# Kernel tuning notes

Measured on AMD Instinct MI355X. Metric: run time of the kernel, lower is better.

## Reference

```python
import jax, jax.numpy as jnp
import numpy as np

D_MODEL = 512
D_INNER = 1024   # expand=2
D_STATE = 16
D_CONV = 4
DT_RANK = 32     # ceil(d_model/16)
N_LAYERS = 3
STATE_DIM = 256
NUM_ACTIONS = 9
BATCH = 8
SEQ = 1024


def setup_inputs() -> dict:
    key = jax.random.key(0)
    ks = iter(jax.random.split(key, 32))
    def nrm(shape, scale=0.02):
        return jax.random.normal(next(ks), shape, jnp.float32) * scale
    inp = {}
    inp["state_sequences"] = jax.random.normal(next(ks), (BATCH, SEQ, STATE_DIM), jnp.float32)
    inp["embed_w"] = nrm((D_MODEL, STATE_DIM), STATE_DIM ** -0.5)
    inp["embed_b"] = jnp.zeros((D_MODEL,), jnp.float32)
    inp["in_proj_w"] = nrm((N_LAYERS, 2 * D_INNER, D_MODEL), D_MODEL ** -0.5)
    inp["conv_w"] = nrm((N_LAYERS, D_INNER, D_CONV), 0.2)
    inp["conv_b"] = jnp.zeros((N_LAYERS, D_INNER), jnp.float32)
    inp["x_proj_w"] = nrm((N_LAYERS, DT_RANK + 2 * D_STATE, D_INNER), D_INNER ** -0.5)
    inp["dt_proj_w"] = nrm((N_LAYERS, D_INNER, DT_RANK), DT_RANK ** -0.5)
    # bias so that softplus(dt) ~ 0.01 (standard mamba dt init)
    inp["dt_proj_b"] = jnp.full((N_LAYERS, D_INNER), float(np.log(np.expm1(0.01))), jnp.float32)
    # S4D-real init: A_n = n for n = 1..d_state
    inp["A_log"] = jnp.log(jnp.broadcast_to(
        jnp.arange(1, D_STATE + 1, dtype=jnp.float32), (N_LAYERS, D_INNER, D_STATE)))
    inp["D"] = jnp.ones((N_LAYERS, D_INNER), jnp.float32)
    inp["out_proj_w"] = nrm((N_LAYERS, D_MODEL, D_INNER), D_INNER ** -0.5)
    inp["head1_w"] = nrm((D_MODEL // 2, D_MODEL), D_MODEL ** -0.5)
    inp["head1_b"] = jnp.zeros((D_MODEL // 2,), jnp.float32)
    inp["head2_w"] = nrm((NUM_ACTIONS, D_MODEL // 2), (D_MODEL // 2) ** -0.5)
    inp["head2_b"] = jnp.zeros((NUM_ACTIONS,), jnp.float32)
    return inp


def _mamba_block(x, in_w, cw, cb, xw, dtw, dtb, A_log, Dp, ow):
    """One mamba-ssm Mamba layer (d_inner=2*d_model, d_state=16, d_conv=4)."""
    B, L, _ = x.shape
    xz = jnp.einsum('bld,ed->ble', x, in_w)            # (B,L,2*d_inner)
    xi, z = jnp.split(xz, 2, axis=-1)
    # causal depthwise conv1d along time
    xc = jnp.pad(xi, ((0, 0), (D_CONV - 1, 0), (0, 0)))
    conv = jax.lax.conv_general_dilated(
        xc.transpose(0, 2, 1), cw[:, None, :], (1,), 'VALID',
        feature_group_count=D_INNER)                   # (B,d_inner,L)
    xi = jax.nn.silu(conv.transpose(0, 2, 1) + cb)     # (B,L,d_inner)
    dbl = jnp.einsum('bld,ed->ble', xi, xw)            # (B,L,dt_rank+2*d_state)
    dt, Bm, Cm = jnp.split(dbl, [DT_RANK, DT_RANK + D_STATE], axis=-1)
    dt = jax.nn.softplus(jnp.einsum('blr,dr->bld', dt, dtw) + dtb)  # (B,L,d_inner)
    A = -jnp.exp(A_log)                                # (d_inner,d_state)

    def step(h, inputs):
        dt_t, x_t, B_t, C_t = inputs                   # (B,di),(B,di),(B,ds),(B,ds)
        dA = jnp.exp(dt_t[:, :, None] * A)             # (B,di,ds)
        h = dA * h + (dt_t * x_t)[:, :, None] * B_t[:, None, :]
        y_t = jnp.einsum('bds,bs->bd', h, C_t)
        return h, y_t

    h0 = jnp.zeros((B, D_INNER, D_STATE), xi.dtype)
    seq = (dt.transpose(1, 0, 2), xi.transpose(1, 0, 2),
           Bm.transpose(1, 0, 2), Cm.transpose(1, 0, 2))
    _, ys = jax.lax.scan(step, h0, seq)                # (L,B,d_inner)
    y = ys.transpose(1, 0, 2) + xi * Dp
    y = y * jax.nn.silu(z)
    return jnp.einsum('bld,ed->ble', y, ow)            # (B,L,d_model)


def reference(state_sequences, embed_w, embed_b, in_proj_w, conv_w, conv_b,
              x_proj_w, dt_proj_w, dt_proj_b, A_log, D, out_proj_w,
              head1_w, head1_b, head2_w, head2_b):
    x = jnp.einsum('bls,ds->bld', state_sequences, embed_w) + embed_b
    for i in range(N_LAYERS):
        x = _mamba_block(x, in_proj_w[i], conv_w[i], conv_b[i], x_proj_w[i],
                         dt_proj_w[i], dt_proj_b[i], A_log[i], D[i], out_proj_w[i])
    h = jax.nn.relu(jnp.einsum('bd,hd->bh', x[:, -1, :], head1_w) + head1_b)
    logits = jnp.einsum('bh,ah->ba', h, head2_w) + head2_b  # (B,num_actions)
    return logits
```

## Files before the change

### kernel.cpp

```cpp
#include <hip/hip_runtime.h>
#include <cstdint>
#include <cstddef>


#define DEVI static __device__ __forceinline__

using short8 = __attribute__((ext_vector_type(8))) short;
using f32x4  = __attribute__((ext_vector_type(4))) float;
typedef unsigned short ushort;
typedef unsigned int uint;

extern "C" __device__ float __ocml_native_exp2_f32(float);
DEVI float exp2n_(float x) { return __ocml_native_exp2_f32(x); }

DEVI float sigmoidf_(float x) { return 1.f / (1.f + __expf(-x)); }
DEVI float siluf_(float x)    { return x * sigmoidf_(x); }
DEVI float softplusf_(float x){ return fmaxf(x, 0.f) + log1pf(expf(-fabsf(x))); }

DEVI ushort rne_bf16(float f) {
    uint u = __float_as_uint(f);
    return (ushort)((u + 0x7fffu + ((u >> 16) & 1u)) >> 16);
}
DEVI float bf16_to_f(ushort h) { return __uint_as_float(((uint)h) << 16); }
DEVI uint pack_hl(float v) {
    const ushort hv = rne_bf16(v);
    const ushort lv = rne_bf16(v - bf16_to_f(hv));
    return (uint)hv | ((uint)lv << 16);
}

DEVI void swz_block(int& bx, int& by, int gx, int gy) {
    const int total = gx * gy;
    const int q = total >> 3;
    const int id = by * gx + bx;
    const int s = (id & 7) * q + (id >> 3);
    bx = s % gx;
    by = s / gx;
}

constexpr int LC = 32;
constexpr int NC = 32;
constexpr int PF = 4;
constexpr float LOG2E = 1.44269504f;

DEVI void cvt4(const float4 v, ushort* h, ushort* l) {
    const float vv[4] = {v.x, v.y, v.z, v.w};
    #pragma unroll
    for (int e = 0; e < 4; e++) {
        const ushort hh = rne_bf16(vv[e]);
        h[e] = hh;
        l[e] = rne_bf16(vv[e] - bf16_to_f(hh));
    }
}

__global__ __launch_bounds__(256)
void wcvt_gi_kernel(const float* __restrict__ src, ushort* __restrict__ hi,
                    ushort* __restrict__ lo, int N, int K)
{
    const int idx = blockIdx.x * 256 + threadIdx.x;
    if (idx >= N * (K >> 3)) return;
    const int g = idx / N;
    const int n = idx - g * N;
    const float4 v0 = *reinterpret_cast<const float4*>(&src[(size_t)n * K + g * 8]);
    const float4 v1 = *reinterpret_cast<const float4*>(&src[(size_t)n * K + g * 8 + 4]);
    ushort h[8], l[8];
    cvt4(v0, h, l);
    cvt4(v1, h + 4, l + 4);
    short8 h8, l8;
    #pragma unroll
    for (int e = 0; e < 8; e++) { h8[e] = (short)h[e]; l8[e] = (short)l[e]; }
    *reinterpret_cast<short8*>(&hi[(size_t)idx * 8]) = h8;
    *reinterpret_cast<short8*>(&lo[(size_t)idx * 8]) = l8;
}

__global__ __launch_bounds__(256)
void wcvt3_kernel(const float* __restrict__ s_in, const float* __restrict__ s_out,
                  const float* __restrict__ s_xp, ushort* __restrict__ dst)
{
    const int idx = blockIdx.x * 256 + threadIdx.x;
    if (idx >= 212992) return;
    if (idx < 131072) {
        const int g = idx >> 11, n = idx & 2047;
        const float* sp = s_in + (size_t)n * 512 + g * 8;
        const float4 v0 = *reinterpret_cast<const float4*>(sp);
        const float4 v1 = *reinterpret_cast<const float4*>(sp + 4);
        ushort h[8], l[8];
        cvt4(v0, h, l); cvt4(v1, h + 4, l + 4);
        short8 h8, l8;
        #pragma unroll
        for (int e = 0; e < 8; e++) { h8[e] = (short)h[e]; l8[e] = (short)l[e]; }
        *reinterpret_cast<short8*>(&dst[(size_t)idx * 8]) = h8;
        *reinterpret_cast<short8*>(&dst[1048576 + (size_t)idx * 8]) = l8;
    } else if (idx < 196608) {
        const int j = idx - 131072;
        const int g = j >> 9, n = j & 511;
        const float* sp = s_out + (size_t)n * 1024 + g * 8;
        const float4 v0 = *reinterpret_cast<const float4*>(sp);
        const float4 v1 = *reinterpret_cast<const float4*>(sp + 4);
        ushort h[8], l[8];
        cvt4(v0, h, l); cvt4(v1, h + 4, l + 4);
        short8 h8, l8;
        #pragma unroll
        for (int e = 0; e < 8; e++) { h8[e] = (short)h[e]; l8[e] = (short)l[e]; }
        *reinterpret_cast<short8*>(&dst[2097152 + (size_t)j * 8]) = h8;
        *reinterpret_cast<short8*>(&dst[2621440 + (size_t)j * 8]) = l8;
    } else {
        const int j = idx - 196608;
        const int loc = j * 4;
        const float4 v = *reinterpret_cast<const float4*>(&s_xp[loc]);
        ushort h[4], l[4];
        cvt4(v, h, l);
        *reinterpret_cast<ushort4*>(&dst[3145728 + loc]) = make_ushort4(h[0], h[1], h[2], h[3]);
        *reinterpret_cast<ushort4*>(&dst[3211264 + loc]) = make_ushort4(l[0], l[1], l[2], l[3]);
    }
}

template<int ACT, int AMODE, bool OPACK>
__global__ __launch_bounds__(256)
void gemm_mfma(const float* __restrict__ A, const uint* __restrict__ Apk,
               int lda,
               const ushort* __restrict__ Whi, const ushort* __restrict__ Wlo,
               int Wn, const float* __restrict__ bias,
               float* C, float* C2, int nsplit,
               uint* __restrict__ Cpk, int ldc, int K)
{
    __shared__ short As_hi[4096], As_lo[4096];

    int bx = blockIdx.x, by = blockIdx.y;
    swz_block(bx, by, gridDim.x, gridDim.y);

    const int tid  = threadIdx.x;
    const int lane = tid & 63;
    const int wave = tid >> 6;
    const int wr   = wave >> 1;
    const int wc   = wave & 1;
    const int row0 = by * 128;
    const int col0 = bx * 128;

    const int g  = tid & 3;
    const int r0 = tid >> 2;

    const int lg = lane >> 4;
    const int lm = lane & 15;
    const int chA = lg * 128 + ((wr * 64 + lm) ^ lg);

    f32x4 acc[4][4];
    #pragma unroll
    for (int i = 0; i < 4; i++)
        #pragma unroll
        for (int j = 0; j < 4; j++) acc[i][j] = (f32x4){0.f, 0.f, 0.f, 0.f};

    float4 av0[2], av1[2];
    uint4  au0[2], au1[2];

    auto gloadA = [&](int k0) {
        #pragma unroll
        for (int p = 0; p < 2; p++) {
            const int rr = r0 + p * 64;
            if constexpr (AMODE == 1) {
                const uint* ap = Apk + (size_t)(row0 + rr) * lda + k0 + g * 8;
                au0[p] = *reinterpret_cast<const uint4*>(ap);
                au1[p] = *reinterpret_cast<const uint4*>(ap + 4);
            } else {
                const float* ap = A + (size_t)(row0 + rr) * lda + k0 + g * 8;
                av0[p] = *reinterpret_cast<const float4*>(ap);
                av1[p] = *reinterpret_cast<const float4*>(ap + 4);
            }
        }
    };

    gloadA(0);

    for (int k0 = 0; k0 < K; k0 += 32) {
        #pragma unroll
        for (int p = 0; p < 2; p++) {
            const int ch = g * 128 + ((r0 + p * 64) ^ g);
            short8 h8, l8;
            if constexpr (AMODE == 1) {
                uint u[8];
                *reinterpret_cast<uint4*>(u)     = au0[p];
                *reinterpret_cast<uint4*>(u + 4) = au1[p];
                uint* hp = reinterpret_cast<uint*>(&h8);
                uint* lp = reinterpret_cast<uint*>(&l8);
                #pragma unroll
                for (int e = 0; e < 4; e++) {
                    hp[e] = __builtin_amdgcn_perm(u[2*e+1], u[2*e], 0x05040100u);
                    lp[e] = __builtin_amdgcn_perm(u[2*e+1], u[2*e], 0x07060302u);
                }
            } else {
                ushort h[8], l[8];
                cvt4(av0[p], h, l);
                cvt4(av1[p], h + 4, l + 4);
                #pragma unroll
                for (int e = 0; e < 8; e++) { h8[e] = (short)h[e]; l8[e] = (short)l[e]; }
            }
            *reinterpret_cast<short8*>(&As_hi[ch * 8]) = h8;
            *reinterpret_cast<short8*>(&As_lo[ch * 8]) = l8;
        }
        if (k0 + 32 < K) gloadA(k0 + 32);

        short8 b_hi[4], b_lo[4];
        {
            const size_t gkb = (size_t)((k0 >> 3) + lg) * Wn + col0 + wc * 64 + lm;
            #pragma unroll
            for (int j = 0; j < 4; j++) {
                const size_t wo = (gkb + j * 16) * 8;
                b_hi[j] = *reinterpret_cast<const short8*>(&Whi[wo]);
                b_lo[j] = *reinterpret_cast<const short8*>(&Wlo[wo]);
            }
        }
        __syncthreads();

        short8 a_hi[4], a_lo[4];
        #pragma unroll
        for (int i = 0; i < 4; i++) {
            a_hi[i] = *reinterpret_cast<const short8*>(&As_hi[(chA + i * 16) * 8]);
            a_lo[i] = *reinterpret_cast<const short8*>(&As_lo[(chA + i * 16) * 8]);
        }
        #pragma unroll
        for (int i = 0; i < 4; i++)
            #pragma unroll
            for (int j = 0; j < 4; j++) {
                acc[i][j] = __builtin_amdgcn_mfma_f32_16x16x32_bf16(a_hi[i], b_hi[j], acc[i][j], 0, 0, 0);
                acc[i][j] = __builtin_amdgcn_mfma_f32_16x16x32_bf16(a_hi[i], b_lo[j], acc[i][j], 0, 0, 0);
                acc[i][j] = __builtin_amdgcn_mfma_f32_16x16x32_bf16(a_lo[i], b_hi[j], acc[i][j], 0, 0, 0);
            }
        __syncthreads();
    }

    float* Cw = C;
    int cofs = 0;
    if (C2 != nullptr && col0 >= nsplit) { Cw = C2; cofs = nsplit; }

    #pragma unroll
    for (int i = 0; i < 4; i++) {
        const int grow = row0 + wr * 64 + i * 16 + lg * 4;
        #pragma unroll
        for (int j = 0; j < 4; j++) {
            const int gcol = col0 + wc * 64 + j * 16 + lm;
            float bv = 0.f;
            if constexpr (ACT >= 1) bv = bias[gcol];
            #pragma unroll
            for (int r = 0; r < 4; r++) {
                const float v = acc[i][j][r] + bv;
                if constexpr (OPACK) {
                    Cpk[(size_t)(grow + r) * ldc + gcol] = pack_hl(v);
                } else {
                    Cw[(size_t)(grow + r) * ldc + (gcol - cofs)] = v;
                }
            }
        }
    }
}

__global__ __launch_bounds__(256)
void gemm_mfma_xp(const float* __restrict__ A,
                  const ushort* __restrict__ Whi,
                  const ushort* __restrict__ Wlo,
                  float* __restrict__ P)
{
    __shared__ short As_hi[2048], As_lo[2048], Ws_hi[2048], Ws_lo[2048];

    int bx = blockIdx.x, by = blockIdx.y;
    swz_block(bx, by, gridDim.x, gridDim.y);

    const int tid  = threadIdx.x;
    const int lane = tid & 63;
    const int wave = tid >> 6;
    const int wr   = wave >> 1;
    const int wc   = wave & 1;
    const int row0 = bx * 64;
    const int kp   = by;

    const int g = tid & 3;
    const int r = tid >> 2;
    const int ch_st = g * 64 + (r ^ g);

    const int lg = lane >> 4;
    const int lm = lane & 15;

    f32x4 acc[2][2];
    #pragma unroll
    for (int i = 0; i < 2; i++)
        #pragma unroll
        for (int j = 0; j < 2; j++) acc[i][j] = (f32x4){0.f, 0.f, 0.f, 0.f};

    for (int ks = 0; ks < 4; ks++) {
        const int kbase = kp * 128 + ks * 32;
        __syncthreads();
        {
            const float* ap = A + (size_t)(row0 + r) * 1024 + kbase + g * 8;
            const float4 v0 = *reinterpret_cast<const float4*>(ap);
            const float4 v1 = *reinterpret_cast<const float4*>(ap + 4);
            ushort h[8], l[8];
            cvt4(v0, h, l);
            cvt4(v1, h + 4, l + 4);
            short8 h8, l8;
            #pragma unroll
            for (int e = 0; e < 8; e++) { h8[e] = (short)h[e]; l8[e] = (short)l[e]; }
            *reinterpret_cast<short8*>(&As_hi[ch_st * 8]) = h8;
            *reinterpret_cast<short8*>(&As_lo[ch_st * 8]) = l8;
        }
        {
            const size_t wo = (size_t)r * 1024 + kbase + g * 8;
            *reinterpret_cast<short8*>(&Ws_hi[ch_st * 8]) =
                *reinterpret_cast<const short8*>(&Whi[wo]);
            *reinterpret_cast<short8*>(&Ws_lo[ch_st * 8]) =
                *reinterpret_cast<const short8*>(&Wlo[wo]);
        }
        __syncthreads();

        short8 a_hi[2], a_lo[2], b_hi[2], b_lo[2];
        #pragma unroll
        for (int i = 0; i < 2; i++) {
            const int ch = lg * 64 + ((wr * 32 + i * 16 + lm) ^ lg);
            a_hi[i] = *reinterpret_cast<const short8*>(&As_hi[ch * 8]);
            a_lo[i] = *reinterpret_cast<const short8*>(&As_lo[ch * 8]);
        }
        #pragma unroll
        for (int j = 0; j < 2; j++) {
            const int ch = lg * 64 + ((wc * 32 + j * 16 + lm) ^ lg);
            b_hi[j] = *reinterpret_cast<const short8*>(&Ws_hi[ch * 8]);
            b_lo[j] = *reinterpret_cast<const short8*>(&Ws_lo[ch * 8]);
        }
        #pragma unroll
        for (int i = 0; i < 2; i++)
            #pragma unroll
            for (int j = 0; j < 2; j++) {
                acc[i][j] = __builtin_amdgcn_mfma_f32_16x16x32_bf16(a_hi[i], b_hi[j], acc[i][j], 0, 0, 0);
                acc[i][j] = __builtin_amdgcn_mfma_f32_16x16x32_bf16(a_hi[i], b_lo[j], acc[i][j], 0, 0, 0);
                acc[i][j] = __builtin_amdgcn_mfma_f32_16x16x32_bf16(a_lo[i], b_hi[j], acc[i][j], 0, 0, 0);
            }
    }

    #pragma unroll
    for (int i = 0; i < 2; i++) {
        const int grow = row0 + wr * 32 + i * 16 + lg * 4;
        #pragma unroll
        for (int j = 0; j < 2; j++) {
            const int gcol = wc * 32 + j * 16 + lm;
            #pragma unroll
            for (int rr = 0; rr < 4; rr++)
                P[((size_t)kp * 8192 + grow + rr) * 64 + gcol] = acc[i][j][rr];
        }
    }
}

__global__ __launch_bounds__(256)
void xp_reduce(const float* __restrict__ P, float* __restrict__ dbl)
{
    const int idx = blockIdx.x * 256 + threadIdx.x;
    float s = 0.f;
    #pragma unroll
    for (int p = 0; p < 8; p++) s += P[(size_t)p * 524288 + idx];
    dbl[idx] = s;
}

__global__ __launch_bounds__(256)
void conv_silu_kernel(const float* __restrict__ xpre,
                      const float* __restrict__ cw,
                      const float* __restrict__ cb,
                      float* __restrict__ xi)
{
    const int idx = blockIdx.x * 256 + threadIdx.x;
    const int d = idx & 1023;
    const int l = (idx >> 10) & 1023;
    const int b = idx >> 20;

    const float4 w = reinterpret_cast<const float4*>(cw)[d];
    float acc = cb[d];
    const float* base = xpre + (size_t)b * 1024 * 1024 + d;
    if (l >= 3) acc = fmaf(base[(size_t)(l - 3) * 1024], w.x, acc);
    if (l >= 2) acc = fmaf(base[(size_t)(l - 2) * 1024], w.y, acc);
    if (l >= 1) acc = fmaf(base[(size_t)(l - 1) * 1024], w.z, acc);
    acc = fmaf(base[(size_t)l * 1024], w.w, acc);
    xi[idx] = siluf_(acc);
}

__global__ __launch_bounds__(256)
void dt_kernel(const float* __restrict__ dbl,
               const float* __restrict__ dtw,
               const float* __restrict__ dtb,
               float* __restrict__ dtout)
{
    __shared__ float S[LC][32];
    const int tid = threadIdx.x;
    const int d   = blockIdx.x * 256 + tid;
    const int c   = blockIdx.y;
    const int b   = blockIdx.z;
    const int t0  = c * LC;

    {
        const int t = tid >> 3, q = tid & 7;
        *reinterpret_cast<float4*>(&S[t][q * 4]) =
            *reinterpret_cast<const float4*>(&dbl[((size_t)b * 1024 + t0 + t) * 64 + q * 4]);
    }
    __syncthreads();

    float W[32];
    #pragma unroll
    for (int q = 0; q < 8; q++)
        *reinterpret_cast<float4*>(&W[q * 4]) =
            *reinterpret_cast<const float4*>(&dtw[(size_t)d * 32 + q * 4]);
    const float bias = dtb[d];

    float* dto = dtout + ((size_t)b * 1024 + t0) * 1024 + d;
    #pragma unroll 4
    for (int t = 0; t < LC; t++) {
        float a0 = bias, a1 = 0.f, a2 = 0.f, a3 = 0.f;
        #pragma unroll
        for (int q = 0; q < 8; q += 4) {
            const float4 s0 = *reinterpret_cast<const float4*>(&S[t][q * 4]);
            const float4 s1 = *reinterpret_cast<const float4*>(&S[t][q * 4 + 4]);
            a0 = fmaf(W[q*4+0], s0.x, a0); a1 = fmaf(W[q*4+1], s0.y, a1);
            a2 = fmaf(W[q*4+2], s0.z, a2); a3 = fmaf(W[q*4+3], s0.w, a3);
            a0 = fmaf(W[q*4+4], s1.x, a0); a1 = fmaf(W[q*4+5], s1.y, a1);
            a2 = fmaf(W[q*4+6], s1.z, a2); a3 = fmaf(W[q*4+7], s1.w, a3);
        }
        dto[(size_t)t * 1024] = softplusf_((a0 + a1) + (a2 + a3));
    }
}

__global__ __launch_bounds__(256)
void scan_p1(const float* __restrict__ xi,
             const float* __restrict__ dtin,
             const float* __restrict__ dbl,
             const float* __restrict__ A_log,
             float* __restrict__ hend,
             float* __restrict__ dtsum)
{
    __shared__ float S[LC][16];
    const int tid  = threadIdx.x;
    const int lane = tid & 63;
    const int wave = tid >> 6;
    const int dloc = lane & 31;
    const int half = lane >> 5;
    const int d    = blockIdx.x * 128 + wave * 32 + dloc;
    const int c    = blockIdx.y;
    const int b    = blockIdx.z;
    const int t0   = c * LC;

    if (tid < 128) {
        const int t = tid >> 2, q = tid & 3;
        *reinterpret_cast<float4*>(&S[t][q * 4]) =
            *reinterpret_cast<const float4*>(&dbl[((size_t)b * 1024 + t0 + t) * 64 + 32 + q * 4]);
    }
    __syncthreads();

    const float A2b = -__expf(A_log[d * 16]) * LOG2E;
    float h[8];
    #pragma unroll
    for (int s = 0; s < 8; s++) h[s] = 0.f;
    float dts = 0.f;

    const float* xi_p = xi   + ((size_t)b * 1024 + t0) * 1024 + d;
    const float* dt_p = dtin + ((size_t)b * 1024 + t0) * 1024 + d;

    float x0[PF], d0[PF], x1[PF], d1[PF], x2[PF], d2[PF];

    auto load = [&](int bt, float (&nx)[PF], float (&nd)[PF]) {
        #pragma unroll
        for (int j = 0; j < PF; j++) {
            const size_t tt = (size_t)(bt * PF + j);
            nx[j] = xi_p[tt * 1024];
            nd[j] = dt_p[tt * 1024];
        }
    };
    auto comp = [&](int bt, float (&cx)[PF], float (&cd)[PF]) {
        #pragma unroll
        for (int j = 0; j < PF; j++) {
            const int t = bt * PF + j;
            const float dtv = cd[j];
            dts += dtv;
            const float dx = dtv * cx[j];
            const float E  = exp2n_(dtv * A2b);
            const float E2 = E * E;
            const float E4 = E2 * E2;
            const float E8 = E4 * E4;
            float p = half ? E8 * E : E;
            const float4 B0 = *reinterpret_cast<const float4*>(&S[t][half * 8]);
            const float4 B1 = *reinterpret_cast<const float4*>(&S[t][half * 8 + 4]);
            h[0] = fmaf(p, h[0], dx * B0.x); p *= E;
            h[1] = fmaf(p, h[1], dx * B0.y); p *= E;
            h[2] = fmaf(p, h[2], dx * B0.z); p *= E;
            h[3] = fmaf(p, h[3], dx * B0.w); p *= E;
            h[4] = fmaf(p, h[4], dx * B1.x); p *= E;
            h[5] = fmaf(p, h[5], dx * B1.y); p *= E;
            h[6] = fmaf(p, h[6], dx * B1.z); p *= E;
            h[7] = fmaf(p, h[7], dx * B1.w);
        }
    };

    load(0, x0, d0); load(1, x1, d1);
    load(2, x2, d2); comp(0, x0, d0);
    load(3, x0, d0); comp(1, x1, d1);
    load(4, x1, d1); comp(2, x2, d2);
    load(5, x2, d2); comp(3, x0, d0);
    load(6, x0, d0); comp(4, x1, d1);
    load(7, x1, d1); comp(5, x2, d2);
    comp(6, x0, d0);
    comp(7, x1, d1);

    float* hp = hend + (((size_t)b * NC + c) * 1024 + d) * 16 + half * 8;
    *reinterpret_cast<float4*>(&hp[0]) = *reinterpret_cast<const float4*>(&h[0]);
    *reinterpret_cast<float4*>(&hp[4]) = *reinterpret_cast<const float4*>(&h[4]);
    if (half == 0) dtsum[((size_t)b * NC + c) * 1024 + d] = dts;
}

__global__ __launch_bounds__(256)
void scan_p2(float* __restrict__ hbuf,
             const float* __restrict__ dtsum,
             const float* __restrict__ A_log)
{
    const int gid = blockIdx.x * 256 + threadIdx.x;
    const int s = gid & 15;
    const int d = (gid >> 4) & 1023;
    const int b = gid >> 14;

    const float A2 = -__expf(A_log[d * 16 + s]) * LOG2E;
    float h = 0.f;
    #pragma unroll
    for (int c = 0; c < NC; c++) {
        const size_t idx = (((size_t)b * NC + c) * 1024 + d) * 16 + s;
        const float he = hbuf[idx];
        const float aP = exp2n_(A2 * dtsum[((size_t)b * NC + c) * 1024 + d]);
        hbuf[idx] = h;
        h = fmaf(aP, h, he);
    }
}

__global__ __launch_bounds__(256)
void scan_p3(const float* __restrict__ xi,
             float* dtio,
             const float* __restrict__ dbl,
             const float* __restrict__ zbuf,
             const float* __restrict__ A_log,
             const float* __restrict__ Dp,
             const float* __restrict__ h0)
{
    __shared__ float S[LC][32];
    const int tid  = threadIdx.x;
    const int lane = tid & 63;
    const int wave = tid >> 6;
    const int dloc = lane & 31;
    const int half = lane >> 5;
    const int d    = blockIdx.x * 128 + wave * 32 + dloc;
    const int c    = blockIdx.y;
    const int b    = blockIdx.z;
    const int t0   = c * LC;

    {
        const int t = tid >> 3, q = tid & 7;
        *reinterpret_cast<float4*>(&S[t][q * 4]) =
            *reinterpret_cast<const float4*>(&dbl[((size_t)b * 1024 + t0 + t) * 64 + 32 + q * 4]);
    }
    __syncthreads();

    const float A2b = -__expf(A_log[d * 16]) * LOG2E;
    float h[8];
    const float* h0p = h0 + (((size_t)b * NC + c) * 1024 + d) * 16 + half * 8;
    *reinterpret_cast<float4*>(&h[0]) = *reinterpret_cast<const float4*>(&h0p[0]);
    *reinterpret_cast<float4*>(&h[4]) = *reinterpret_cast<const float4*>(&h0p[4]);

    const float Dv = Dp[d];
    const size_t rowbase = ((size_t)b * 1024 + t0) * 1024 + d;
    const float* xi_p = xi + rowbase;
    const float* dt_p = dtio + rowbase;
    const float* z_p  = zbuf + rowbase;
    uint* ypk_p = reinterpret_cast<uint*>(dtio) + rowbase;

    float x0[PF], z0[PF], d0[PF], x1[PF], z1[PF], d1[PF], x2[PF], z2[PF], d2[PF];

    auto load = [&](int bt, float (&nx)[PF], float (&nz)[PF], float (&nd)[PF]) {
        #pragma unroll
        for (int j = 0; j < PF; j++) {
            const size_t tt = (size_t)(bt * PF + j);
            nx[j] = xi_p[tt * 1024];
            nz[j] = z_p[tt * 1024];
            nd[j] = dt_p[tt * 1024];
        }
    };
    auto comp = [&](int bt, float (&cx)[PF], float (&cz)[PF], float (&cd)[PF]) {
        #pragma unroll
        for (int j = 0; j < PF; j++) {
            const int t = bt * PF + j;
            const float dtv = cd[j];
            const float dx  = dtv * cx[j];
            const float E  = exp2n_(dtv * A2b);
            const float E2 = E * E;
            const float E4 = E2 * E2;
            const float E8 = E4 * E4;
            float p = half ? E8 * E : E;
            const float4 B0 = *reinterpret_cast<const float4*>(&S[t][half * 8]);
            const float4 B1 = *reinterpret_cast<const float4*>(&S[t][half * 8 + 4]);
            const float4 C0 = *reinterpret_cast<const float4*>(&S[t][16 + half * 8]);
            const float4 C1 = *reinterpret_cast<const float4*>(&S[t][16 + half * 8 + 4]);
            float y = 0.f;
            h[0] = fmaf(p, h[0], dx * B0.x); y = fmaf(h[0], C0.x, y); p *= E;
            h[1] = fmaf(p, h[1], dx * B0.y); y = fmaf(h[1], C0.y, y); p *= E;
            h[2] = fmaf(p, h[2], dx * B0.z); y = fmaf(h[2], C0.z, y); p *= E;
            h[3] = fmaf(p, h[3], dx * B0.w); y = fmaf(h[3], C0.w, y); p *= E;
            h[4] = fmaf(p, h[4], dx * B1.x); y = fmaf(h[4], C1.x, y); p *= E;
            h[5] = fmaf(p, h[5], dx * B1.y); y = fmaf(h[5], C1.y, y); p *= E;
            h[6] = fmaf(p, h[6], dx * B1.z); y = fmaf(h[6], C1.z, y); p *= E;
            h[7] = fmaf(p, h[7], dx * B1.w); y = fmaf(h[7], C1.w, y);
            const float yfull = y + __shfl_xor(y, 32);
            if (half == 0) {
                const float yv = (yfull + cx[j] * Dv) * siluf_(cz[j]);
                ypk_p[(size_t)t * 1024] = pack_hl(yv);
            }
        }
    };

    load(0, x0, z0, d0); load(1, x1, z1, d1);
    load(2, x2, z2, d2); comp(0, x0, z0, d0);
    load(3, x0, z0, d0); comp(1, x1, z1, d1);
    load(4, x1, z1, d1); comp(2, x2, z2, d2);
    load(5, x2, z2, d2); comp(3, x0, z0, d0);
    load(6, x0, z0, d0); comp(4, x1, z1, d1);
    load(7, x1, z1, d1); comp(5, x2, z2, d2);
    comp(6, x0, z0, d0);
    comp(7, x1, z1, d1);
}

__global__ __launch_bounds__(256)
void head1_kernel(const uint* __restrict__ xpk,
                  const float* __restrict__ w,
                  const float* __restrict__ bias,
                  float* __restrict__ hh)
{
    const int tid = threadIdx.x;
    const int jl  = tid >> 4;
    const int ks  = tid & 15;
    const int j   = blockIdx.x * 16 + jl;

    const float* wr = w + (size_t)j * 512 + ks * 32;
    float acc[8];
    #pragma unroll
    for (int b = 0; b < 8; b++) {
        const size_t ro = ((size_t)b * 1024 + 1023) * 512 + ks * 32;
        float a = 0.f;
        #pragma unroll
        for (int k = 0; k < 32; k += 4) {
            const float4 wv = *reinterpret_cast<const float4*>(&wr[k]);
            const uint4  pv = *reinterpret_cast<const uint4*>(&xpk[ro + k]);
            a = fmaf(wv.x, bf16_to_f((ushort)(pv.x & 0xffff)) + bf16_to_f((ushort)(pv.x >> 16)), a);
            a = fmaf(wv.y, bf16_to_f((ushort)(pv.y & 0xffff)) + bf16_to_f((ushort)(pv.y >> 16)), a);
            a = fmaf(wv.z, bf16_to_f((ushort)(pv.z & 0xffff)) + bf16_to_f((ushort)(pv.z >> 16)), a);
            a = fmaf(wv.w, bf16_to_f((ushort)(pv.w & 0xffff)) + bf16_to_f((ushort)(pv.w >> 16)), a);
        }
        acc[b] = a;
    }
    #pragma unroll
    for (int b = 0; b < 8; b++) {
        float p = acc[b];
        p += __shfl_xor(p, 1);
        p += __shfl_xor(p, 2);
        p += __shfl_xor(p, 4);
        p += __shfl_xor(p, 8);
        if (ks == 0) hh[b * 256 + j] = fmaxf(p + bias[j], 0.f);
    }
}

__global__ void head2_kernel(const float* __restrict__ hh,
                             const float* __restrict__ w,
                             const float* __restrict__ b2,
                             float* __restrict__ out)
{
    const int t = threadIdx.x;
    if (t < 72) {
        const int bb = t / 9, a = t % 9;
        const float* hr = hh + bb * 256;
        const float* wr = w + a * 256;
        float acc = b2[a];
        for (int jj = 0; jj < 256; jj++) acc = fmaf(hr[jj], wr[jj], acc);
        out[t] = acc;
    }
}


extern "C" void kernel_launch(void* const* d_in, const int* in_sizes, int n_in,
                              void* d_out, int out_size, void* d_ws, size_t ws_size,
                              hipStream_t stream)
{
    const float* state     = (const float*)d_in[0];
    const float* embed_w   = (const float*)d_in[1];
    const float* embed_b   = (const float*)d_in[2];
    const float* in_proj_w = (const float*)d_in[3];
    const float* conv_w    = (const float*)d_in[4];
    const float* conv_b    = (const float*)d_in[5];
    const float* x_proj_w  = (const float*)d_in[6];
    const float* dt_proj_w = (const float*)d_in[7];
    const float* dt_proj_b = (const float*)d_in[8];
    const float* A_log     = (const float*)d_in[9];
    const float* Dp        = (const float*)d_in[10];
    const float* out_proj_w= (const float*)d_in[11];
    const float* h1w       = (const float*)d_in[12];
    const float* h1b       = (const float*)d_in[13];
    const float* h2w       = (const float*)d_in[14];
    const float* h2b       = (const float*)d_in[15];
    float* out = (float*)d_out;

    float* reg0 = (float*)d_ws;
    uint*  xpk  = (uint*)reg0;
    float* dblp = reg0;
    float* hbuf = reg0;

    float* xpre = reg0 + (size_t)8192 * 512;
    float* zbuf = xpre + (size_t)8192 * 1024;
    float* xi   = zbuf + (size_t)8192 * 1024;
    float* dtbf = xi   + (size_t)8192 * 1024;
    float* dbl  = dtbf + (size_t)8192 * 1024;
    float* hh   = dbl  + (size_t)8192 * 64;
    ushort* wl = (ushort*)(hh + 2048);
    ushort* we_hi = wl + 3276800;
    ushort* we_lo = we_hi + 131072;
    float* dtsum = (float*)(we_lo + 131072);

    uint* ypk = (uint*)dtbf;

    const dim3 blk(256);

    wcvt_gi_kernel<<<dim3(64), blk, 0, stream>>>(embed_w, we_hi, we_lo, 512, 256);
    gemm_mfma<1, 0, true><<<dim3(4, 64), blk, 0, stream>>>(
        state, nullptr, 256, we_hi, we_lo, 512, embed_b,
        nullptr, nullptr, 0, xpk, 512, 256);

    for (int i = 0; i < 3; i++) {
        const float* Alog_i = A_log + (size_t)i * 1024 * 16;
        const float* dtw_i  = dt_proj_w + (size_t)i * 1024 * 32;
        const float* dtb_i  = dt_proj_b + (size_t)i * 1024;

        wcvt3_kernel<<<dim3(832), blk, 0, stream>>>(
            in_proj_w + (size_t)i * 2048 * 512,
            out_proj_w + (size_t)i * 512 * 1024,
            x_proj_w + (size_t)i * 64 * 1024, wl);

        gemm_mfma<0, 1, false><<<dim3(16, 64), blk, 0, stream>>>(
            nullptr, xpk, 512, wl, wl + 1048576, 2048, nullptr,
            xpre, zbuf, 1024, nullptr, 1024, 512);

        conv_silu_kernel<<<dim3(8 * 1024 * 1024 / 256), blk, 0, stream>>>(
            xpre, conv_w + (size_t)i * 1024 * 4, conv_b + (size_t)i * 1024, xi);

        gemm_mfma_xp<<<dim3(128, 8), blk, 0, stream>>>(
            xi, wl + 3145728, wl + 3211264, dblp);
        xp_reduce<<<dim3(2048), blk, 0, stream>>>(dblp, dbl);

        dt_kernel<<<dim3(4, NC, 8), blk, 0, stream>>>(dbl, dtw_i, dtb_i, dtbf);

        scan_p1<<<dim3(8, NC, 8), blk, 0, stream>>>(
            xi, dtbf, dbl, Alog_i, hbuf, dtsum);
        scan_p2<<<dim3(512), blk, 0, stream>>>(hbuf, dtsum, Alog_i);
        scan_p3<<<dim3(8, NC, 8), blk, 0, stream>>>(
            xi, dtbf, dbl, zbuf, Alog_i, Dp + (size_t)i * 1024, hbuf);

        gemm_mfma<0, 1, true><<<dim3(4, 64), blk, 0, stream>>>(
            nullptr, ypk, 1024, wl + 2097152, wl + 2621440, 512, nullptr,
            nullptr, nullptr, 0, xpk, 512, 1024);
    }

    head1_kernel<<<dim3(16), blk, 0, stream>>>(xpk, h1w, h1b, hh);
    head2_kernel<<<dim3(1), dim3(128), 0, stream>>>(hh, h2w, h2b, out);
}
```

Baseline: 758.3 us.

## Fuse causal conv+SiLU into x_proj GEMM loader and scan kernels

Removes the standalone conv_silu kernel and its 32MB xi intermediate per layer. The x_proj GEMM now loads four shifted rows of xpre and computes conv+SiLU while staging into LDS, and both scan passes recompute conv+SiLU on the fly from a rolling three-element history. This saves one full write and several reads of the activation tensor. In exchange it adds extra global reads of the shifted rows, which mostly hit cache, plus repeated SiLU arithmetic in three kernels.

```diff
diff --git a/kernel.cpp b/kernel.cpp
--- a/kernel.cpp
+++ b/kernel.cpp
@@ -253,7 +253,9 @@
 }
 
 __global__ __launch_bounds__(256)
-void gemm_mfma_xp(const float* __restrict__ A,
+void gemm_mfma_xp(const float* __restrict__ xpre,
+                  const float* __restrict__ cw,
+                  const float* __restrict__ cb,
                   const ushort* __restrict__ Whi,
                   const ushort* __restrict__ Wlo,
                   float* __restrict__ P)
@@ -278,6 +280,9 @@
     const int lg = lane >> 4;
     const int lm = lane & 15;
 
+    const int rg = row0 + r;
+    const int lrow = rg & 1023;
+
     f32x4 acc[2][2];
     #pragma unroll
     for (int i = 0; i < 2; i++)
@@ -288,15 +293,33 @@
         const int kbase = kp * 128 + ks * 32;
         __syncthreads();
         {
-            const float* ap = A + (size_t)(row0 + r) * 1024 + kbase + g * 8;
-            const float4 v0 = *reinterpret_cast<const float4*>(ap);
-            const float4 v1 = *reinterpret_cast<const float4*>(ap + 4);
-            ushort h[8], l[8];
-            cvt4(v0, h, l);
-            cvt4(v1, h + 4, l + 4);
+            const int dbase = kbase + g * 8;
+            const float* xr = xpre + (size_t)rg * 1024 + dbase;
+            float xv[8], m1[8], m2[8], m3[8];
+            *reinterpret_cast<float4*>(&xv[0]) = *reinterpret_cast<const float4*>(xr);
+            *reinterpret_cast<float4*>(&xv[4]) = *reinterpret_cast<const float4*>(xr + 4);
+            const float4 z4 = {0.f, 0.f, 0.f, 0.f};
+            *reinterpret_cast<float4*>(&m1[0]) = (lrow >= 1) ? *reinterpret_cast<const float4*>(xr - 1024) : z4;
+            *reinterpret_cast<float4*>(&m1[4]) = (lrow >= 1) ? *reinterpret_cast<const float4*>(xr - 1024 + 4) : z4;
+            *reinterpret_cast<float4*>(&m2[0]) = (lrow >= 2) ? *reinterpret_cast<const float4*>(xr - 2048) : z4;
+            *reinterpret_cast<float4*>(&m2[4]) = (lrow >= 2) ? *reinterpret_cast<const float4*>(xr - 2048 + 4) : z4;
+            *reinterpret_cast<float4*>(&m3[0]) = (lrow >= 3) ? *reinterpret_cast<const float4*>(xr - 3072) : z4;
+            *reinterpret_cast<float4*>(&m3[4]) = (lrow >= 3) ? *reinterpret_cast<const float4*>(xr - 3072 + 4) : z4;
+
             short8 h8, l8;
             #pragma unroll
-            for (int e = 0; e < 8; e++) { h8[e] = (short)h[e]; l8[e] = (short)l[e]; }
+            for (int e = 0; e < 8; e++) {
+                const float4 cwe = reinterpret_cast<const float4*>(cw)[dbase + e];
+                float a = cb[dbase + e];
+                a = fmaf(m3[e], cwe.x, a);
+                a = fmaf(m2[e], cwe.y, a);
+                a = fmaf(m1[e], cwe.z, a);
+                a = fmaf(xv[e], cwe.w, a);
+                const float s = siluf_(a);
+                const ushort hv = rne_bf16(s);
+                h8[e] = (short)hv;
+                l8[e] = (short)rne_bf16(s - bf16_to_f(hv));
+            }
             *reinterpret_cast<short8*>(&As_hi[ch_st * 8]) = h8;
             *reinterpret_cast<short8*>(&As_lo[ch_st * 8]) = l8;
         }
@@ -356,27 +379,6 @@
 }
 
 __global__ __launch_bounds__(256)
-void conv_silu_kernel(const float* __restrict__ xpre,
-                      const float* __restrict__ cw,
-                      const float* __restrict__ cb,
-                      float* __restrict__ xi)
-{
-    const int idx = blockIdx.x * 256 + threadIdx.x;
-    const int d = idx & 1023;
-    const int l = (idx >> 10) & 1023;
-    const int b = idx >> 20;
-
-    const float4 w = reinterpret_cast<const float4*>(cw)[d];
-    float acc = cb[d];
-    const float* base = xpre + (size_t)b * 1024 * 1024 + d;
-    if (l >= 3) acc = fmaf(base[(size_t)(l - 3) * 1024], w.x, acc);
-    if (l >= 2) acc = fmaf(base[(size_t)(l - 2) * 1024], w.y, acc);
-    if (l >= 1) acc = fmaf(base[(size_t)(l - 1) * 1024], w.z, acc);
-    acc = fmaf(base[(size_t)l * 1024], w.w, acc);
-    xi[idx] = siluf_(acc);
-}
-
-__global__ __launch_bounds__(256)
 void dt_kernel(const float* __restrict__ dbl,
                const float* __restrict__ dtw,
                const float* __restrict__ dtb,
@@ -421,10 +423,12 @@
 }
 
 __global__ __launch_bounds__(256)
-void scan_p1(const float* __restrict__ xi,
+void scan_p1(const float* __restrict__ xpre,
              const float* __restrict__ dtin,
              const float* __restrict__ dbl,
              const float* __restrict__ A_log,
+             const float* __restrict__ cw,
+             const float* __restrict__ cb,
              float* __restrict__ hend,
              float* __restrict__ dtsum)
 {
@@ -447,13 +451,23 @@
     __syncthreads();
 
     const float A2b = -__expf(A_log[d * 16]) * LOG2E;
+    const float4 cwv = reinterpret_cast<const float4*>(cw)[d];
+    const float cbv = cb[d];
     float h[8];
     #pragma unroll
     for (int s = 0; s < 8; s++) h[s] = 0.f;
     float dts = 0.f;
 
-    const float* xi_p = xi   + ((size_t)b * 1024 + t0) * 1024 + d;
-    const float* dt_p = dtin + ((size_t)b * 1024 + t0) * 1024 + d;
+    const size_t rowbase = ((size_t)b * 1024 + t0) * 1024 + d;
+    const float* xp_p = xpre + rowbase;
+    const float* dt_p = dtin + rowbase;
+
+    float xm1 = 0.f, xm2 = 0.f, xm3 = 0.f;
+    if (c > 0) {
+        xm1 = xp_p[-1024];
+        xm2 = xp_p[-2048];
+        xm3 = xp_p[-3072];
+    }
 
     float x0[PF], d0[PF], x1[PF], d1[PF], x2[PF], d2[PF];
 
@@ -461,7 +475,7 @@
         #pragma unroll
         for (int j = 0; j < PF; j++) {
             const size_t tt = (size_t)(bt * PF + j);
-            nx[j] = xi_p[tt * 1024];
+            nx[j] = xp_p[tt * 1024];
             nd[j] = dt_p[tt * 1024];
         }
     };
@@ -469,9 +483,17 @@
         #pragma unroll
         for (int j = 0; j < PF; j++) {
             const int t = bt * PF + j;
+            float a = cbv;
+            a = fmaf(xm3, cwv.x, a);
+            a = fmaf(xm2, cwv.y, a);
+            a = fmaf(xm1, cwv.z, a);
+            a = fmaf(cx[j], cwv.w, a);
+            const float xiv = siluf_(a);
+            xm3 = xm2; xm2 = xm1; xm1 = cx[j];
+
             const float dtv = cd[j];
             dts += dtv;
-            const float dx = dtv * cx[j];
+            const float dx = dtv * xiv;
             const float E  = exp2n_(dtv * A2b);
             const float E2 = E * E;
             const float E4 = E2 * E2;
@@ -529,11 +551,13 @@
 }
 
 __global__ __launch_bounds__(256)
-void scan_p3(const float* __restrict__ xi,
+void scan_p3(const float* __restrict__ xpre,
              float* dtio,
              const float* __restrict__ dbl,
              const float* __restrict__ zbuf,
              const float* __restrict__ A_log,
+             const float* __restrict__ cw,
+             const float* __restrict__ cb,
              const float* __restrict__ Dp,
              const float* __restrict__ h0)
 {
@@ -556,6 +580,8 @@
     __syncthreads();
 
     const float A2b = -__expf(A_log[d * 16]) * LOG2E;
+    const float4 cwv = reinterpret_cast<const float4*>(cw)[d];
+    const float cbv = cb[d];
     float h[8];
     const float* h0p = h0 + (((size_t)b * NC + c) * 1024 + d) * 16 + half * 8;
     *reinterpret_cast<float4*>(&h[0]) = *reinterpret_cast<const float4*>(&h0p[0]);
@@ -563,18 +589,25 @@
 
     const float Dv = Dp[d];
     const size_t rowbase = ((size_t)b * 1024 + t0) * 1024 + d;
-    const float* xi_p = xi + rowbase;
+    const float* xp_p = xpre + rowbase;
     const float* dt_p = dtio + rowbase;
     const float* z_p  = zbuf + rowbase;
     uint* ypk_p = reinterpret_cast<uint*>(dtio) + rowbase;
 
+    float xm1 = 0.f, xm2 = 0.f, xm3 = 0.f;
+    if (c > 0) {
+        xm1 = xp_p[-1024];
+        xm2 = xp_p[-2048];
+        xm3 = xp_p[-3072];
+    }
+
     float x0[PF], z0[PF], d0[PF], x1[PF], z1[PF], d1[PF], x2[PF], z2[PF], d2[PF];
 
     auto load = [&](int bt, float (&nx)[PF], float (&nz)[PF], float (&nd)[PF]) {
         #pragma unroll
         for (int j = 0; j < PF; j++) {
             const size_t tt = (size_t)(bt * PF + j);
-            nx[j] = xi_p[tt * 1024];
+            nx[j] = xp_p[tt * 1024];
             nz[j] = z_p[tt * 1024];
             nd[j] = dt_p[tt * 1024];
         }
@@ -583,8 +616,16 @@
         #pragma unroll
         for (int j = 0; j < PF; j++) {
             const int t = bt * PF + j;
+            float a = cbv;
+            a = fmaf(xm3, cwv.x, a);
+            a = fmaf(xm2, cwv.y, a);
+            a = fmaf(xm1, cwv.z, a);
+            a = fmaf(cx[j], cwv.w, a);
+            const float xiv = siluf_(a);
+            xm3 = xm2; xm2 = xm1; xm1 = cx[j];
+
             const float dtv = cd[j];
-            const float dx  = dtv * cx[j];
+            const float dx  = dtv * xiv;
             const float E  = exp2n_(dtv * A2b);
             const float E2 = E * E;
             const float E4 = E2 * E2;
@@ -605,7 +646,7 @@
             h[7] = fmaf(p, h[7], dx * B1.w); y = fmaf(h[7], C1.w, y);
             const float yfull = y + __shfl_xor(y, 32);
             if (half == 0) {
-                const float yv = (yfull + cx[j] * Dv) * siluf_(cz[j]);
+                const float yv = (yfull + xiv * Dv) * siluf_(cz[j]);
                 ypk_p[(size_t)t * 1024] = pack_hl(yv);
             }
         }
@@ -729,6 +770,8 @@
         const float* Alog_i = A_log + (size_t)i * 1024 * 16;
         const float* dtw_i  = dt_proj_w + (size_t)i * 1024 * 32;
         const float* dtb_i  = dt_proj_b + (size_t)i * 1024;
+        const float* cw_i   = conv_w + (size_t)i * 1024 * 4;
+        const float* cb_i   = conv_b + (size_t)i * 1024;
 
         wcvt3_kernel<<<dim3(832), blk, 0, stream>>>(
             in_proj_w + (size_t)i * 2048 * 512,
@@ -739,20 +782,18 @@
             nullptr, xpk, 512, wl, wl + 1048576, 2048, nullptr,
             xpre, zbuf, 1024, nullptr, 1024, 512);
 
-        conv_silu_kernel<<<dim3(8 * 1024 * 1024 / 256), blk, 0, stream>>>(
-            xpre, conv_w + (size_t)i * 1024 * 4, conv_b + (size_t)i * 1024, xi);
-
         gemm_mfma_xp<<<dim3(128, 8), blk, 0, stream>>>(
-            xi, wl + 3145728, wl + 3211264, dblp);
+            xpre, cw_i, cb_i, wl + 3145728, wl + 3211264, dblp);
         xp_reduce<<<dim3(2048), blk, 0, stream>>>(dblp, dbl);
 
         dt_kernel<<<dim3(4, NC, 8), blk, 0, stream>>>(dbl, dtw_i, dtb_i, dtbf);
 
         scan_p1<<<dim3(8, NC, 8), blk, 0, stream>>>(
-            xi, dtbf, dbl, Alog_i, hbuf, dtsum);
+            xpre, dtbf, dbl, Alog_i, cw_i, cb_i, hbuf, dtsum);
         scan_p2<<<dim3(512), blk, 0, stream>>>(hbuf, dtsum, Alog_i);
         scan_p3<<<dim3(8, NC, 8), blk, 0, stream>>>(
-            xi, dtbf, dbl, zbuf, Alog_i, Dp + (size_t)i * 1024, hbuf);
+            xpre, dtbf, dbl, zbuf, Alog_i, cw_i, cb_i,
+            Dp + (size_t)i * 1024, hbuf);
 
         gemm_mfma<0, 1, true><<<dim3(4, 64), blk, 0, stream>>>(
             nullptr, ypk, 1024, wl + 2097152, wl + 2621440, 512, nullptr,
```

New measurement: 812.6 us. 1.07x slower.
